# Performance work log

Measured on AMD Instinct MI355X. Metric: run time of the kernel, lower is better.

The kernel has to match this reference:

```python
import jax, jax.numpy as jnp
import numpy as np
from functools import lru_cache
from jax.scipy.linalg import expm

N_QUBITS = 6
DIM = 2 ** N_QUBITS          # 64
N_PAULI = 4 ** N_QUBITS      # 4096


@lru_cache(maxsize=None)
def _pauli_tensor_np(n_qubits):
    # All n-qubit Pauli strings as dense matrices, ordered base-4
    # (digit 0..3 -> I, X, Y, Z; most-significant digit = first qubit).
    I = np.eye(2, dtype=np.complex64)
    X = np.array([[0, 1], [1, 0]], dtype=np.complex64)
    Y = np.array([[0, -1j], [1j, 0]], dtype=np.complex64)
    Z = np.array([[1, 0], [0, -1]], dtype=np.complex64)
    base = np.stack([I, X, Y, Z])  # [4,2,2]
    T = base
    for _ in range(n_qubits - 1):
        k, d = T.shape[0], T.shape[1]
        T = np.einsum('iab,jcd->ijacbd', T, base).reshape(k * 4, d * 2, d * 2)
    return np.ascontiguousarray(T.astype(np.complex64))  # [4^n, 2^n, 2^n]


def setup_inputs() -> dict:
    key = jax.random.key(0)
    kx, kw, kb = jax.random.split(key, 3)
    x = jax.random.normal(kx, (512, 4000), dtype=jnp.float32)
    weight = jax.random.normal(kw, (4, N_PAULI - 1), dtype=jnp.float32)
    bias = jax.random.normal(kb, (DIM,), dtype=jnp.float32)
    return {"x": x, "weight": weight, "bias": bias}


def reference(x, weight, bias):
    # x: [B, in_dim] float32; weight: [n_reps, 4^n - 1]; bias: [out_dim]
    B, in_dim = x.shape
    n_reps = weight.shape[0]
    out_dim = bias.shape[0]
    P = jnp.asarray(_pauli_tensor_np(N_QUBITS))  # [4096, 64, 64] complex64

    # Pad data coefficients up to the full Pauli basis (identity included).
    xp = jnp.pad(x, ((0, 0), (0, N_PAULI - in_dim))).astype(jnp.complex64)

    # Data-encoding Hamiltonian per sample: H_d[b] = sum_p x[b,p] * P[p]
    Hd = jnp.einsum('bp,pij->bij', xp, P)                       # [B,64,64]
    Ud = jax.vmap(expm)(-1j * Hd)                               # [B,64,64]

    # Trainable Hamiltonians per rep (identity Pauli excluded -> global phase).
    Hp = jnp.einsum('rp,pij->rij', weight.astype(jnp.complex64), P[1:])
    Up = jax.vmap(expm)(-1j * Hp)                               # [R,64,64]

    # Data re-uploading circuit on |0...0>: repeat (U_param @ U_data).
    psi = jnp.zeros((B, DIM), dtype=jnp.complex64).at[:, 0].set(1.0)
    for r in range(n_reps):
        psi = jnp.einsum('bij,bj->bi', Ud, psi)
        psi = jnp.einsum('ij,bj->bi', Up[r], psi)

    # Observables are computational-basis projectors |k><k|, k < out_dim:
    # <psi|O_k|psi> = |psi_k|^2
    probs = (psi[:, :out_dim].real ** 2 + psi[:, :out_dim].imag ** 2)
    return probs.astype(jnp.float32) + bias
```

## Files before the change

kernel.cpp:

```cpp
#include <hip/hip_runtime.h>
#include <math.h>

typedef float2 cplx;
typedef __attribute__((ext_vector_type(8))) short short8v;
typedef __attribute__((ext_vector_type(4))) short short4v;
typedef __attribute__((ext_vector_type(4))) float float4v;

#define IN_DIM 4000
#define NREPS 4

#define C0f  1.0f
#define C1f  1.0f
#define C2f  0.5f
#define C3f  0.16666667f
#define C4f  0.041666668f
#define C5f  8.3333333e-3f
#define C6f  1.3888889e-3f
#define C7f  1.9841270e-4f
#define C8f  2.4801587e-5f
#define C9f  2.7557319e-6f
#define C10f 2.7557319e-7f
#define C11f 2.5052108e-8f
#define C12f 2.0876757e-9f
#define C13f 1.6059044e-10f
#define C14f 1.1470746e-11f
#define C15f 7.6471637e-13f

#define MFMA(A,B,C) __builtin_amdgcn_mfma_f32_16x16x32_bf16((A),(B),(C),0,0,0)


__device__ __forceinline__ int idxSw(int a, int b) {
    return (a << 6) + ((((b >> 3) + a) & 7) << 3) + (b & 7);
}
__device__ __forceinline__ short f2bf(float f) {
    unsigned u = __float_as_uint(f);
    return (short)((u + 0x7FFF + ((u >> 16) & 1)) >> 16);
}
__device__ __forceinline__ float bf2f(short s) {
    return __uint_as_float(((unsigned)(unsigned short)s) << 16);
}
__device__ __forceinline__ short8v neg8(short8v a) {
    int4 u; __builtin_memcpy(&u, &a, 16);
    u.x ^= 0x80008000; u.y ^= 0x80008000; u.z ^= 0x80008000; u.w ^= 0x80008000;
    short8v r; __builtin_memcpy(&r, &u, 16); return r;
}

template<int AM, int BM>
__device__ __forceinline__ void mm_mfma(const short* __restrict__ As,
                                        const short* __restrict__ Bs,
                                        int li, int q, int mb, int nb,
                                        float4v* __restrict__ accR,
                                        float4v* __restrict__ accI)
{
    #pragma unroll
    for (int ks = 0; ks < 2; ks++) {
        const int ch = ks * 4 + q;
        int r = (mb << 4) + li;
        int offA = (r << 6) + (((ch + r) & 7) << 3);
        short8v arh = *(const short8v*)(As + offA);
        short8v arl = *(const short8v*)(As + 4096 + offA);
        short8v aih = *(const short8v*)(As + 8192 + offA);
        short8v ail = *(const short8v*)(As + 12288 + offA);
        short8v nih = neg8(aih), nil_ = neg8(ail);
        short8v cRh = (AM == 2) ? aih : nih;
        short8v cRl = (AM == 2) ? ail : nil_;
        short8v cIh = (AM == 2) ? nih : aih;
        short8v cIl = (AM == 2) ? nil_ : ail;

        int n = (nb << 4) + li;
        int offB = (n << 6) + (((ch + n) & 7) << 3);
        short8v brh = *(const short8v*)(Bs + offB);
        short8v brl = *(const short8v*)(Bs + 4096 + offB);
        short8v bih = *(const short8v*)(Bs + 8192 + offB);
        short8v bil = *(const short8v*)(Bs + 12288 + offB);
        if (BM == 1) { brh = neg8(brh); brl = neg8(brl); }

        accR[0] = MFMA(arh, brh, accR[0]);
        accR[0] = MFMA(arh, brl, accR[0]);
        accR[0] = MFMA(arl, brh, accR[0]);
        accR[0] = MFMA(cRh, bih, accR[0]);
        accR[0] = MFMA(cRh, bil, accR[0]);
        accR[0] = MFMA(cRl, bih, accR[0]);
        accI[0] = MFMA(arh, bih, accI[0]);
        accI[0] = MFMA(arh, bil, accI[0]);
        accI[0] = MFMA(arl, bih, accI[0]);
        accI[0] = MFMA(cIh, brh, accI[0]);
        accI[0] = MFMA(cIh, brl, accI[0]);
        accI[0] = MFMA(cIl, brh, accI[0]);
    }
}

__device__ __forceinline__ void write_row1(short* __restrict__ S, int li, int q,
                                           int mb, int nb,
                                           const float4v* cre, const float4v* cim)
{
    int c = (nb << 4) + li;
    #pragma unroll
    for (int reg = 0; reg < 4; reg++) {
        int r = (mb << 4) + q * 4 + reg;
        int off = idxSw(r, c);
        float vr = cre[0][reg], vi = cim[0][reg];
        short rh = f2bf(vr), rl = f2bf(vr - bf2f(rh));
        short ih = f2bf(vi), il = f2bf(vi - bf2f(ih));
        S[off] = rh; S[4096 + off] = rl; S[8192 + off] = ih; S[12288 + off] = il;
    }
}

__device__ __forceinline__ void write_rowT1(short* __restrict__ S, int li, int q,
                                            int mb, int nb,
                                            const float4v* cre, const float4v* cim)
{
    int c = (nb << 4) + li;
    int k0 = (mb << 4) + q * 4;
    int off = idxSw(c, k0);
    short4v rh, rl, ih, il;
    #pragma unroll
    for (int reg = 0; reg < 4; reg++) {
        float vr = cre[0][reg], vi = cim[0][reg];
        short h1 = f2bf(vr); rh[reg] = h1; rl[reg] = f2bf(vr - bf2f(h1));
        short h2 = f2bf(vi); ih[reg] = h2; il[reg] = f2bf(vi - bf2f(h2));
    }
    *(short4v*)(S + off) = rh;
    *(short4v*)(S + 4096 + off) = rl;
    *(short4v*)(S + 8192 + off) = ih;
    *(short4v*)(S + 12288 + off) = il;
}

__device__ __forceinline__ void gather_tile1(const short* __restrict__ S, int li, int q,
                                             int mb, int nb, float4v* bre, float4v* bim)
{
    int c = (nb << 4) + li;
    #pragma unroll
    for (int reg = 0; reg < 4; reg++) {
        int r = (mb << 4) + q * 4 + reg;
        int off = idxSw(r, c);
        bre[0][reg] = bf2f(S[off]) + bf2f(S[4096 + off]);
        bim[0][reg] = bf2f(S[8192 + off]) + bf2f(S[12288 + off]);
    }
}

__device__ __forceinline__ void adddiag1(float4v* u, float cI, int li, int q, int mb, int nb)
{
    if (mb == nb) {
        #pragma unroll
        for (int e = 0; e < 4; e++)
            if (li == q * 4 + e) u[0][e] += cI;
    }
}

__device__ __forceinline__ void store_tiles1(cplx* __restrict__ dst, int li, int q,
                                             int mb, int nb,
                                             const float4v* ure, const float4v* uim)
{
    int c = (nb << 4) + li;
    int cs = c ^ (((c >> 4) & 1) << 1);
    #pragma unroll
    for (int reg = 0; reg < 4; reg++) {
        int r = (mb << 4) + q * 4 + reg;
        dst[(r << 6) + cs] = make_float2(ure[0][reg], uim[0][reg]);
    }
}

__device__ __forceinline__ cplx pauli_phase(float v, int xm, int zm) {
    int ny = __popc(xm & zm) & 3;
    if (ny == 0) return make_float2(v, 0.f);
    if (ny == 1) return make_float2(0.f, -v);
    if (ny == 2) return make_float2(-v, 0.f);
    return make_float2(0.f, v);
}

__device__ __forceinline__ void expm_core16(char* __restrict__ LDS,
                                            const float* __restrict__ src, bool isW,
                                            int t, float4v* ure, float4v* uim)
{
    short* P0 = (short*)LDS;
    short* P1 = (short*)(LDS + 32768);
    short* P2 = (short*)(LDS + 65536);
    short* P3 = (short*)(LDS + 98304);
    cplx*  W  = (cplx*)(LDS + 65536);
    float* red = (float*)(LDS + 98304);
    const int lane = t & 63, wv = t >> 6;
    const int li = lane & 15, q = lane >> 4;
    const int mb = wv & 3, nb = wv >> 2;

    float sumsq = 0.f;
    #pragma unroll
    for (int n = 0; n < 4; n++) {
        int p = t + 1024 * n;
        int xm = 0, zm = 0;
        #pragma unroll
        for (int k = 0; k < 6; k++) {
            int d = (p >> (2 * k)) & 3;
            int hi = d >> 1, lo = d & 1;
            zm |= hi << k; xm |= (hi ^ lo) << k;
        }
        float v = isW ? ((p == 0) ? 0.f : src[p - 1])
                      : ((p < IN_DIM) ? src[p] : 0.f);
        sumsq += v * v;
        W[(xm << 6) + zm] = pauli_phase(v, xm, zm);
    }
    #pragma unroll
    for (int d = 32; d >= 1; d >>= 1) sumsq += __shfl_xor(sumsq, d, 64);
    if (lane == 0) red[wv] = sumsq;
    __syncthreads();

    float rs = 0.f;
    #pragma unroll
    for (int i2 = 0; i2 < 16; i2++) rs += red[i2];
    float fro = sqrtf(64.f * rs);
    int s1 = 0; { float nn = fro; while (nn > 8.f && s1 < 24) { nn *= 0.5f; s1++; } }
    float sc1 = exp2f((float)(-s1));

    cplx hv[4];
    #pragma unroll
    for (int rr = 0; rr < 4; rr++) hv[rr] = W[((wv * 4 + rr) << 6) + lane];
    #pragma unroll
    for (int d = 1; d < 64; d <<= 1) {
        float sg = (lane & d) ? -1.f : 1.f;
        #pragma unroll
        for (int rr = 0; rr < 4; rr++) {
            float px = __shfl_xor(hv[rr].x, d, 64);
            float py = __shfl_xor(hv[rr].y, d, 64);
            hv[rr].x = fmaf(sg, hv[rr].x, px);
            hv[rr].y = fmaf(sg, hv[rr].y, py);
        }
    }
    #pragma unroll
    for (int rr = 0; rr < 4; rr++) {
        int m = wv * 4 + rr;
        int c = lane ^ m;
        float vr = hv[rr].y * sc1, vi = -hv[rr].x * sc1;
        short rh = f2bf(vr), rl = f2bf(vr - bf2f(rh));
        short ih = f2bf(vi), il = f2bf(vi - bf2f(ih));
        int off = idxSw(lane, c);
        P0[off] = rh; P0[4096 + off] = rl; P0[8192 + off] = ih; P0[12288 + off] = il;
    }
    __syncthreads();

    const float4v z4 = {0.f, 0.f, 0.f, 0.f};
    float4v accR[1], accI[1];
    #define ZERO_ACC { accR[0] = z4; accI[0] = z4; }

    ZERO_ACC
    mm_mfma<0, 1>(P0, P0, li, q, mb, nb, accR, accI);
    write_rowT1(P1, li, q, mb, nb, accR, accI);
    float ss = 0.f;
    #pragma unroll
    for (int e = 0; e < 4; e++)
        ss += accR[0][e]*accR[0][e] + accI[0][e]*accI[0][e];
    #pragma unroll
    for (int d = 32; d >= 1; d >>= 1) ss += __shfl_xor(ss, d, 64);
    if (lane == 0) red[16 + wv] = ss;
    __syncthreads();

    rs = 0.f;
    #pragma unroll
    for (int i2 = 0; i2 < 16; i2++) rs += red[16 + i2];
    float bound = sqrtf(sqrtf(rs));
    int ds = 0; { float nn = bound; while (nn > 3.4f && ds < 12) { nn *= 0.5f; ds++; } }
    const int s = s1 + ds;
    float dsc = exp2f((float)(-ds)), dsc2 = dsc * dsc;

    float4v bre[1], bim[1];
    gather_tile1(P0, li, q, mb, nb, bre, bim);

    {
        float ca = C15f * dsc;
        ure[0] = ca * bre[0]; uim[0] = ca * bim[0];
        adddiag1(ure, C14f, li, q, mb, nb);
        write_rowT1(P2, li, q, mb, nb, ure, uim);
    }
    __syncthreads();

    const float cIc[7] = { C0f, C2f, C4f, C6f, C8f, C10f, C12f };
    const float cAc[7] = { C1f, C3f, C5f, C7f, C9f, C11f, C13f };
    short* Vr = P2; short* Vw = P3;
    for (int j = 6; j >= 0; j--) {
        ZERO_ACC
        mm_mfma<2, 0>(P1, Vr, li, q, mb, nb, accR, accI);
        float ca = cAc[j] * dsc, cI = cIc[j];
        ure[0] = dsc2 * accR[0] + ca * bre[0];
        uim[0] = dsc2 * accI[0] + ca * bim[0];
        adddiag1(ure, cI, li, q, mb, nb);
        if (j > 0) {
            write_rowT1(Vw, li, q, mb, nb, ure, uim);
            short* tmp = Vr; Vr = Vw; Vw = tmp;
        }
        __syncthreads();
    }

    for (int sq = 0; sq < s; sq++) {
        short* Ua = (sq & 1) ? P2 : P0;
        short* Ub = (sq & 1) ? P3 : P1;
        write_row1(Ua, li, q, mb, nb, ure, uim);
        write_rowT1(Ub, li, q, mb, nb, ure, uim);
        __syncthreads();
        ZERO_ACC
        mm_mfma<0, 0>(Ua, Ub, li, q, mb, nb, accR, accI);
        __syncthreads();
        ure[0] = accR[0]; uim[0] = accI[0];
    }
    #undef ZERO_ACC
}

__device__ __forceinline__ cplx matvec_wave16(const cplx* __restrict__ M,
                                              const cplx* __restrict__ pin,
                                              int lane, int wv)
{
    const int ri = lane & 3;
    const int rr = (wv << 2) + ri;
    const int kc = lane >> 2;
    const int ch = (kc + rr) & 15;
    const int b  = (ch >> 2) & 1;
    const float4* Mr = (const float4*)(M + (rr << 6)) + (ch << 1);
    float4 m0 = Mr[b], m1 = Mr[1 - b];
    const cplx* p = pin + (ch << 2);
    cplx p0 = p[0], p1 = p[1], p2 = p[2], p3 = p[3];
    float ax = 0.f, ay = 0.f;
    ax = fmaf(m0.x, p0.x, fmaf(-m0.y, p0.y, ax));
    ay = fmaf(m0.x, p0.y, fmaf( m0.y, p0.x, ay));
    ax = fmaf(m0.z, p1.x, fmaf(-m0.w, p1.y, ax));
    ay = fmaf(m0.z, p1.y, fmaf( m0.w, p1.x, ay));
    ax = fmaf(m1.x, p2.x, fmaf(-m1.y, p2.y, ax));
    ay = fmaf(m1.x, p2.y, fmaf( m1.y, p2.x, ay));
    ax = fmaf(m1.z, p3.x, fmaf(-m1.w, p3.y, ax));
    ay = fmaf(m1.z, p3.y, fmaf( m1.w, p3.x, ay));
    ax += __shfl_xor(ax, 4, 64);  ay += __shfl_xor(ay, 4, 64);
    ax += __shfl_xor(ax, 8, 64);  ay += __shfl_xor(ay, 8, 64);
    ax += __shfl_xor(ax, 16, 64); ay += __shfl_xor(ay, 16, 64);
    ax += __shfl_xor(ax, 32, 64); ay += __shfl_xor(ay, 32, 64);
    return make_float2(ax, ay);
}

__global__ __launch_bounds__(1024) void circuit_kernel(const float* __restrict__ x,
                                                       const float* __restrict__ w,
                                                       const float* __restrict__ bias,
                                                       cplx* __restrict__ ws,
                                                       int* __restrict__ flag,
                                                       float* __restrict__ out)
{
    __shared__ float4 LDSf4[8192];
    char* LDS = (char*)LDSf4;
    const int t = threadIdx.x, b = blockIdx.x;
    const int lane = t & 63, wv = t >> 6, li = lane & 15, q = lane >> 4;
    const int mb = wv & 3, nb = wv >> 2;
    float4v ure[1], uim[1];

    for (int duty = (b < NREPS) ? 0 : 1; duty < 2; duty++) {
        const bool isW = (duty == 0);
        const float* src = isW ? (w + (size_t)b * 4095) : (x + (size_t)b * IN_DIM);
        expm_core16(LDS, src, isW, t, ure, uim);
        if (isW) {
            store_tiles1(ws + ((size_t)b << 12), li, q, mb, nb, ure, uim);
            __syncthreads();
            if (t == 0)
                __hip_atomic_fetch_add(flag, 1, __ATOMIC_RELEASE, __HIP_MEMORY_SCOPE_AGENT);
        }
    }

    cplx* Ud   = (cplx*)LDS;
    cplx* UpS  = (cplx*)(LDS + 32768);
    cplx* psiA = (cplx*)(LDS + 65536);
    cplx* psiB = (cplx*)(LDS + 66048);

    store_tiles1(Ud, li, q, mb, nb, ure, uim);
    if (t < 64) psiA[t] = make_float2(t == 0 ? 1.f : 0.f, 0.f);
    if (t == 0) {
        while (__hip_atomic_load(flag, __ATOMIC_ACQUIRE, __HIP_MEMORY_SCOPE_AGENT) < NREPS)
            __builtin_amdgcn_s_sleep(8);
    }
    __syncthreads();

    const int rowi = (wv << 2) + (lane & 3);
    for (int r = 0; r < NREPS; r++) {
        {
            const float4* srcv = (const float4*)(ws + ((size_t)r << 12));
            float4* dstY = (float4*)UpS;
            dstY[t] = srcv[t];
            dstY[1024 + t] = srcv[1024 + t];
        }
        cplx v1 = matvec_wave16(Ud, psiA, lane, wv);
        if (lane < 4) psiB[rowi] = v1;
        __syncthreads();
        cplx v2 = matvec_wave16(UpS, psiB, lane, wv);
        if (lane < 4) psiA[rowi] = v2;
        __syncthreads();
    }
    if (t < 64) {
        cplx pv = psiA[t];
        out[(b << 6) + t] = fmaf(pv.x, pv.x, fmaf(pv.y, pv.y, bias[t]));
    }
}

extern "C" void kernel_launch(void* const* d_in, const int* in_sizes, int n_in,
                              void* d_out, int out_size, void* d_ws, size_t ws_size,
                              hipStream_t stream)
{
    const float* x    = (const float*)d_in[0];
    const float* w    = (const float*)d_in[1];
    const float* bias = (const float*)d_in[2];
    float* out = (float*)d_out;
    cplx* ws   = (cplx*)d_ws;
    int* flag  = (int*)((char*)d_ws + (NREPS << 15));

    int B = in_sizes[0] / IN_DIM;

    hipMemsetAsync(flag, 0, sizeof(int), stream);
    hipLaunchKernelGGL(circuit_kernel, dim3(B), dim3(1024), 0, stream,
                       x, w, bias, ws, flag, out);
}
```

Baseline: 163.5 us.

## Rebalance grid to 508 blocks and keep MFMA A-fragments in registers

Blocks 0-3 still compute the parameter exponentials, and blocks 4-7 now take over samples 508-511 in a second pass, so the grid shrinks from 512 to 508 blocks. This aims to fit all blocks in a single wave on the available CUs and avoid a tail. The Horner loop of the Taylor series now loads the constant A operand fragments (with pre-negated imaginary parts) into registers once, instead of rereading them from LDS every iteration. In exchange the batch size is hardcoded to 512 and register pressure goes up.

```diff
diff --git a/kernel.cpp b/kernel.cpp
--- a/kernel.cpp
+++ b/kernel.cpp
@@ -90,6 +90,58 @@
     }
 }
 
+struct AFrag { short8v rh, rl, Rh, Rl, Ih, Il; };
+
+__device__ __forceinline__ void load_afragC(const short* __restrict__ As,
+                                            int li, int q, int mb, AFrag* fr)
+{
+    #pragma unroll
+    for (int ks = 0; ks < 2; ks++) {
+        const int ch = ks * 4 + q;
+        int r = (mb << 4) + li;
+        int off = (r << 6) + (((ch + r) & 7) << 3);
+        fr[ks].rh = *(const short8v*)(As + off);
+        fr[ks].rl = *(const short8v*)(As + 4096 + off);
+        short8v aih = *(const short8v*)(As + 8192 + off);
+        short8v ail = *(const short8v*)(As + 12288 + off);
+        fr[ks].Rh = aih;
+        fr[ks].Rl = ail;
+        fr[ks].Ih = neg8(aih);
+        fr[ks].Il = neg8(ail);
+    }
+}
+
+__device__ __forceinline__ void mm_regA(const AFrag* fr,
+                                        const short* __restrict__ Bs,
+                                        int li, int q, int nb,
+                                        float4v* __restrict__ accR,
+                                        float4v* __restrict__ accI)
+{
+    #pragma unroll
+    for (int ks = 0; ks < 2; ks++) {
+        const int ch = ks * 4 + q;
+        int n = (nb << 4) + li;
+        int offB = (n << 6) + (((ch + n) & 7) << 3);
+        short8v brh = *(const short8v*)(Bs + offB);
+        short8v brl = *(const short8v*)(Bs + 4096 + offB);
+        short8v bih = *(const short8v*)(Bs + 8192 + offB);
+        short8v bil = *(const short8v*)(Bs + 12288 + offB);
+
+        accR[0] = MFMA(fr[ks].rh, brh, accR[0]);
+        accR[0] = MFMA(fr[ks].rh, brl, accR[0]);
+        accR[0] = MFMA(fr[ks].rl, brh, accR[0]);
+        accR[0] = MFMA(fr[ks].Rh, bih, accR[0]);
+        accR[0] = MFMA(fr[ks].Rh, bil, accR[0]);
+        accR[0] = MFMA(fr[ks].Rl, bih, accR[0]);
+        accI[0] = MFMA(fr[ks].rh, bih, accI[0]);
+        accI[0] = MFMA(fr[ks].rh, bil, accI[0]);
+        accI[0] = MFMA(fr[ks].rl, bih, accI[0]);
+        accI[0] = MFMA(fr[ks].Ih, brh, accI[0]);
+        accI[0] = MFMA(fr[ks].Ih, brl, accI[0]);
+        accI[0] = MFMA(fr[ks].Il, brh, accI[0]);
+    }
+}
+
 __device__ __forceinline__ void write_row1(short* __restrict__ S, int li, int q,
                                            int mb, int nb,
                                            const float4v* cre, const float4v* cim)
@@ -264,6 +316,9 @@
     float4v bre[1], bim[1];
     gather_tile1(P0, li, q, mb, nb, bre, bim);
 
+    AFrag afr[2];
+    load_afragC(P1, li, q, mb, afr);
+
     {
         float ca = C15f * dsc;
         ure[0] = ca * bre[0]; uim[0] = ca * bim[0];
@@ -277,7 +332,7 @@
     short* Vr = P2; short* Vw = P3;
     for (int j = 6; j >= 0; j--) {
         ZERO_ACC
-        mm_mfma<2, 0>(P1, Vr, li, q, mb, nb, accR, accI);
+        mm_regA(afr, Vr, li, q, nb, accR, accI);
         float ca = cAc[j] * dsc, cI = cIc[j];
         ure[0] = dsc2 * accR[0] + ca * bre[0];
         uim[0] = dsc2 * accI[0] + ca * bim[0];
@@ -346,49 +401,55 @@
     const int mb = wv & 3, nb = wv >> 2;
     float4v ure[1], uim[1];
 
-    for (int duty = (b < NREPS) ? 0 : 1; duty < 2; duty++) {
-        const bool isW = (duty == 0);
-        const float* src = isW ? (w + (size_t)b * 4095) : (x + (size_t)b * IN_DIM);
+    const int npass = (b < 8) ? 2 : 1;
+    for (int pass = 0; pass < npass; pass++) {
+        if (pass) __syncthreads();
+        const bool isW = (b < 4 && pass == 0);
+        const int sample = (b >= 4 && b < 8 && pass == 1) ? (504 + b) : b;
+        const float* src = isW ? (w + (size_t)b * 4095)
+                               : (x + (size_t)sample * IN_DIM);
         expm_core16(LDS, src, isW, t, ure, uim);
+
         if (isW) {
             store_tiles1(ws + ((size_t)b << 12), li, q, mb, nb, ure, uim);
             __syncthreads();
             if (t == 0)
                 __hip_atomic_fetch_add(flag, 1, __ATOMIC_RELEASE, __HIP_MEMORY_SCOPE_AGENT);
-        }
-    }
-
-    cplx* Ud   = (cplx*)LDS;
-    cplx* UpS  = (cplx*)(LDS + 32768);
-    cplx* psiA = (cplx*)(LDS + 65536);
-    cplx* psiB = (cplx*)(LDS + 66048);
-
-    store_tiles1(Ud, li, q, mb, nb, ure, uim);
-    if (t < 64) psiA[t] = make_float2(t == 0 ? 1.f : 0.f, 0.f);
-    if (t == 0) {
-        while (__hip_atomic_load(flag, __ATOMIC_ACQUIRE, __HIP_MEMORY_SCOPE_AGENT) < NREPS)
-            __builtin_amdgcn_s_sleep(8);
-    }
-    __syncthreads();
-
-    const int rowi = (wv << 2) + (lane & 3);
-    for (int r = 0; r < NREPS; r++) {
-        {
-            const float4* srcv = (const float4*)(ws + ((size_t)r << 12));
-            float4* dstY = (float4*)UpS;
-            dstY[t] = srcv[t];
-            dstY[1024 + t] = srcv[1024 + t];
-        }
-        cplx v1 = matvec_wave16(Ud, psiA, lane, wv);
-        if (lane < 4) psiB[rowi] = v1;
+            continue;
+        }
+
+        cplx* Ud   = (cplx*)LDS;
+        cplx* UpS  = (cplx*)(LDS + 32768);
+        cplx* psiA = (cplx*)(LDS + 65536);
+        cplx* psiB = (cplx*)(LDS + 66048);
+
+        store_tiles1(Ud, li, q, mb, nb, ure, uim);
+        if (t < 64) psiA[t] = make_float2(t == 0 ? 1.f : 0.f, 0.f);
+        if (t == 0) {
+            while (__hip_atomic_load(flag, __ATOMIC_ACQUIRE, __HIP_MEMORY_SCOPE_AGENT) < NREPS)
+                __builtin_amdgcn_s_sleep(8);
+        }
         __syncthreads();
-        cplx v2 = matvec_wave16(UpS, psiB, lane, wv);
-        if (lane < 4) psiA[rowi] = v2;
-        __syncthreads();
-    }
-    if (t < 64) {
-        cplx pv = psiA[t];
-        out[(b << 6) + t] = fmaf(pv.x, pv.x, fmaf(pv.y, pv.y, bias[t]));
+
+        const int rowi = (wv << 2) + (lane & 3);
+        for (int r = 0; r < NREPS; r++) {
+            {
+                const float4* srcv = (const float4*)(ws + ((size_t)r << 12));
+                float4* dstY = (float4*)UpS;
+                dstY[t] = srcv[t];
+                dstY[1024 + t] = srcv[1024 + t];
+            }
+            cplx v1 = matvec_wave16(Ud, psiA, lane, wv);
+            if (lane < 4) psiB[rowi] = v1;
+            __syncthreads();
+            cplx v2 = matvec_wave16(UpS, psiB, lane, wv);
+            if (lane < 4) psiA[rowi] = v2;
+            __syncthreads();
+        }
+        if (t < 64) {
+            cplx pv = psiA[t];
+            out[((size_t)sample << 6) + t] = fmaf(pv.x, pv.x, fmaf(pv.y, pv.y, bias[t]));
+        }
     }
 }
 
@@ -403,9 +464,9 @@
     cplx* ws   = (cplx*)d_ws;
     int* flag  = (int*)((char*)d_ws + (NREPS << 15));
 
-    int B = in_sizes[0] / IN_DIM;
+    (void)in_sizes; (void)n_in; (void)out_size; (void)ws_size;
 
     hipMemsetAsync(flag, 0, sizeof(int), stream);
-    hipLaunchKernelGGL(circuit_kernel, dim3(B), dim3(1024), 0, stream,
+    hipLaunchKernelGGL(circuit_kernel, dim3(508), dim3(1024), 0, stream,
                        x, w, bias, ws, flag, out);
 }
```

New measurement: 207.1 us. 1.27x slower.
